# Performance work log

Measured on AMD Instinct MI355X. Metric: run time of the kernel, lower is better.

## Reference

```python
import jax, jax.numpy as jnp
import numpy as np

VOCAB, DIM, SEQ, DEPTH, WS, MULT = 32, 256, 8192, 6, 512, 4
BATCH = 2
NEG = -1e9  # mask fill value


def setup_inputs():
    key = jax.random.key(0)
    ks = jax.random.split(key, 8)
    L, d, h = DEPTH, DIM, DIM * MULT
    s = 0.02
    return {
        "tokens": jax.random.randint(ks[0], (BATCH, SEQ), 0, VOCAB),
        "embed": jax.random.normal(ks[1], (VOCAB, d)) * s,
        "ff_ln_s": jnp.ones((L, d)),
        "ff_ln_b": jnp.zeros((L, d)),
        "w1": jax.random.normal(ks[2], (L, d, h)) * s,
        "b1": jnp.zeros((L, h)),
        "w2": jax.random.normal(ks[3], (L, h, d)) * s,
        "b2": jnp.zeros((L, d)),
        "lnf_s": jnp.ones((d,)),
        "lnf_b": jnp.zeros((d,)),
        "w_out": jax.random.normal(ks[4], (d, VOCAB)) * s,
        "b_out": jnp.zeros((VOCAB,)),
    }


def layer_norm(x, s, b, eps=1e-5):
    m = jnp.mean(x, axis=-1, keepdims=True)
    v = jnp.var(x, axis=-1, keepdims=True)
    return (x - m) * jax.lax.rsqrt(v + eps) * s + b


def rotate_half(x):
    x1, x2 = jnp.split(x, 2, axis=-1)
    return jnp.concatenate([-x2, x1], axis=-1)


def local_attn(x, ws):
    # lucidrains LocalAttention: causal, look_backward=1, look_forward=0,
    # exact_windowsize=True, rotary pos emb on q/k. q = k = v = x (no projections).
    b, n, d = x.shape
    inv_freq = 1.0 / (10000.0 ** (jnp.arange(0, d, 2, dtype=jnp.float32) / d))
    t = jnp.arange(n, dtype=jnp.float32)
    fr = t[:, None] * inv_freq[None, :]
    fr = jnp.concatenate([fr, fr], axis=-1)  # (n, d)
    qk = x * jnp.cos(fr) + rotate_half(x) * jnp.sin(fr)  # rotary applied to q and k (identical)
    w = n // ws
    bq = qk.reshape(b, w, ws, d)
    bk = bq  # q == k here
    bv = x.reshape(b, w, ws, d)
    # look_around: each window sees [previous window, current window]
    pk = jnp.pad(bk, ((0, 0), (1, 0), (0, 0), (0, 0)))[:, :-1]
    pv = jnp.pad(bv, ((0, 0), (1, 0), (0, 0), (0, 0)))[:, :-1]
    bk2 = jnp.concatenate([pk, bk], axis=2)  # (b, w, 2*ws, d)
    bv2 = jnp.concatenate([pv, bv], axis=2)
    tq = jnp.arange(n).reshape(w, ws)
    tp = jnp.pad(tq, ((1, 0), (0, 0)), constant_values=-1)[:-1]
    tk = jnp.concatenate([tp, tq], axis=1)  # (w, 2*ws), -1 marks pad
    allowed = (
        (tk[:, None, :] >= 0)
        & (tq[:, :, None] >= tk[:, None, :])          # causal
        & (tq[:, :, None] <= tk[:, None, :] + ws)     # exact windowsize (look_backward=1)
    )
    sim = jnp.einsum("bwid,bwjd->bwij", bq, bk2) * (d ** -0.5)
    sim = jnp.where(allowed[None], sim, NEG)
    attn = jax.nn.softmax(sim, axis=-1)
    out = jnp.einsum("bwij,bwjd->bwid", attn, bv2)
    return out.reshape(b, n, d)


def reference(tokens, embed, ff_ln_s, ff_ln_b, w1, b1, w2, b2, lnf_s, lnf_b, w_out, b_out):
    x = embed[tokens]  # (b, n, d)
    for i in range(DEPTH):
        x = x + local_attn(x, WS)
        h = layer_norm(x, ff_ln_s[i], ff_ln_b[i])
        h = jax.nn.gelu(h @ w1[i] + b1[i], approximate=False)
        x = x + (h @ w2[i] + b2[i])
    return layer_norm(x, lnf_s, lnf_b) @ w_out + b_out  # (b, n, vocab)
```

## Files before the change

kernel.cpp:

```cpp
#include <hip/hip_runtime.h>
#include <hip/hip_bf16.h>
#include <math.h>

#define BATCH 2
#define SEQL 8192
#define DD 256
#define HDIM 1024
#define NLAYER 6
#define WSZ 512
#define NVOCAB 32
#define NTOK (BATCH*SEQL)
#define PLN (DD*HDIM)

typedef unsigned short u16;
typedef __attribute__((ext_vector_type(8))) short bf16x8;
typedef __attribute__((ext_vector_type(4))) float f32x4;

union B8 { uint4 u; bf16x8 b; ushort s[8]; uint w[4]; };

__device__ inline float bf2f(u16 v){
  unsigned int u = ((unsigned int)v) << 16;
  return __uint_as_float(u);
}
__device__ inline u16 f2bf(float f){
  unsigned int u = __float_as_uint(f);
  u += 0x7fff + ((u >> 16) & 1);
  return (u16)(u >> 16);
}

__device__ __forceinline__ void gload16(const void* g, void* l){
  __builtin_amdgcn_global_load_lds(
      (const __attribute__((address_space(1))) unsigned int*)g,
      (__attribute__((address_space(3))) unsigned int*)l, 16, 0, 0);
}

__global__ void k_tables(float* __restrict__ ct, float* __restrict__ st){
  int idx = blockIdx.x * 256 + threadIdx.x;
  if (idx >= SEQL * 128) return;
  int t = idx >> 7, i = idx & 127;
  float freq = expf(-((float)i / 128.0f) * 9.210340371976184f);
  float fr = (float)t * freq;
  ct[idx] = cosf(fr);
  st[idx] = sinf(fr);
}

__global__ void k_embed(const int* __restrict__ tokens, const float* __restrict__ emb,
                        float* __restrict__ x){
  int idx = blockIdx.x * 256 + threadIdx.x;
  int bt = idx >> 6, dv = (idx & 63) << 2;
  int tok = tokens[bt];
  *(float4*)(x + bt * DD + dv) = *(const float4*)(emb + tok * DD + dv);
}

__global__ void k_rope(const float* __restrict__ x, const float* __restrict__ ct,
                       const float* __restrict__ st, u16* __restrict__ qk,
                       u16* __restrict__ xv){
  int idx = blockIdx.x * 256 + threadIdx.x;
  int bt = idx >> 5, iv = (idx & 31) << 2;
  int t = bt & (SEQL - 1);
  const float* xr = x + bt * DD;
  float4 x1 = *(const float4*)(xr + iv);
  float4 x2 = *(const float4*)(xr + 128 + iv);
  float4 c = *(const float4*)(ct + t * 128 + iv);
  float4 s = *(const float4*)(st + t * 128 + iv);
  ushort4 q1, q2, v1, v2;
  q1.x = f2bf(x1.x * c.x - x2.x * s.x);  q2.x = f2bf(x2.x * c.x + x1.x * s.x);
  q1.y = f2bf(x1.y * c.y - x2.y * s.y);  q2.y = f2bf(x2.y * c.y + x1.y * s.y);
  q1.z = f2bf(x1.z * c.z - x2.z * s.z);  q2.z = f2bf(x2.z * c.z + x1.z * s.z);
  q1.w = f2bf(x1.w * c.w - x2.w * s.w);  q2.w = f2bf(x2.w * c.w + x1.w * s.w);
  v1.x = f2bf(x1.x); v1.y = f2bf(x1.y); v1.z = f2bf(x1.z); v1.w = f2bf(x1.w);
  v2.x = f2bf(x2.x); v2.y = f2bf(x2.y); v2.z = f2bf(x2.z); v2.w = f2bf(x2.w);
  *(ushort4*)(qk + bt * DD + iv)       = q1;
  *(ushort4*)(qk + bt * DD + 128 + iv) = q2;
  *(ushort4*)(xv + bt * DD + iv)       = v1;
  *(ushort4*)(xv + bt * DD + 128 + iv) = v2;
}

__global__ void __launch_bounds__(512, 2) k_attn2(const u16* __restrict__ qk,
                                                  const u16* __restrict__ xv,
                                                  const float* __restrict__ x,
                                                  float* __restrict__ y){
  __shared__ char smem[131072];
  float* redbuf = (float*)smem;

  const int tid = threadIdx.x;
  const int lane = tid & 63;
  const int w = tid >> 6;
  const int qh = w >> 1, kh = w & 1;
  const int l15 = lane & 15, lg = lane >> 4;

  const int qb = blockIdx.x * 64;
  const int t0 = qb & (SEQL - 1);
  const size_t bbase = (size_t)(qb >> 13) << 13;

  uint4 qf[8];
  {
    const u16* qr = qk + (size_t)(qb + qh*16 + l15) * DD + lg*4;
    #pragma unroll
    for (int s = 0; s < 8; ++s){
      uint2 a = *(const uint2*)(qr + s*32);
      uint2 b = *(const uint2*)(qr + s*32 + 16);
      qf[s] = make_uint4(a.x, a.y, b.x, b.y);
    }
  }

  f32x4 oacc[16];
  #pragma unroll
  for (int d = 0; d < 16; ++d) oacc[d] = (f32x4){0.f, 0.f, 0.f, 0.f};
  float lacc = 0.f;

  const int p0 = (t0 >= WSZ) ? (t0 - WSZ) : 0;
  const int ntile = ((t0 - p0) >> 6) + 1;

  const int sk15 = tid & 15, skt = (tid >> 4) & 3, sc = tid >> 6;
  const int sdh = tid & 31, sk0 = (tid >> 5) * 4;
  const int vkhw = sk0 >> 5, vh = (sk0 >> 4) & 1, vlgw = (sk0 >> 2) & 3;

  uint4 kreg[4];
  uint  vreg[4][4];

  {
    const u16* sb = qk + (bbase + (size_t)p0 + skt*16 + sk15) * DD;
    #pragma unroll
    for (int u = 0; u < 4; ++u) kreg[u] = *(const uint4*)(sb + u*64 + sc*8);
    #pragma unroll
    for (int u = 0; u < 4; ++u){
      int d0 = sdh*2 + u*64;
      const u16* vb = xv + (bbase + (size_t)p0 + sk0) * DD + d0;
      vreg[u][0] = *(const uint*)(vb);
      vreg[u][1] = *(const uint*)(vb + DD);
      vreg[u][2] = *(const uint*)(vb + 2*DD);
      vreg[u][3] = *(const uint*)(vb + 3*DD);
    }
  }
  #pragma unroll
  for (int u = 0; u < 4; ++u){
    int d0 = u*64 + sc*8;
    int s = d0 >> 5, r = d0 & 31;
    int h = r >> 4, lgw = (r & 15) >> 2;
    int rec = ((s*4 + skt)*4 + lgw)*16 + sk15;
    char* wp = smem + rec*16 + h*8;
    *(uint2*)wp         = make_uint2(kreg[u].x, kreg[u].y);
    *(uint2*)(wp + 256) = make_uint2(kreg[u].z, kreg[u].w);
  }
  #pragma unroll
  for (int u = 0; u < 4; ++u){
    int d0 = sdh*2 + u*64;
    uint a0 = vreg[u][0], a1 = vreg[u][1], a2 = vreg[u][2], a3 = vreg[u][3];
    uint w0 = (a0 & 0xffffu) | (a1 << 16);
    uint w1 = (a2 & 0xffffu) | (a3 << 16);
    uint w2 = (a0 >> 16) | (a1 & 0xffff0000u);
    uint w3 = (a2 >> 16) | (a3 & 0xffff0000u);
    int dimt = d0 >> 4, d15 = d0 & 15;
    int rec = ((dimt*2 + vkhw)*4 + vlgw)*16 + d15;
    char* wp = smem + 32768 + rec*16 + vh*8;
    *(uint2*)wp        = make_uint2(w0, w1);
    *(uint2*)(wp + 16) = make_uint2(w2, w3);
  }
  __syncthreads();

  int cur = 0;
  for (int ti = 0; ti < ntile; ++ti){
    const int p = p0 + ti*64;
    if (ti + 1 < ntile){
      const int pn = p + 64;
      const u16* sb = qk + (bbase + (size_t)pn + skt*16 + sk15) * DD;
      #pragma unroll
      for (int u = 0; u < 4; ++u) kreg[u] = *(const uint4*)(sb + u*64 + sc*8);
      #pragma unroll
      for (int u = 0; u < 4; ++u){
        int d0 = sdh*2 + u*64;
        const u16* vb = xv + (bbase + (size_t)pn + sk0) * DD + d0;
        vreg[u][0] = *(const uint*)(vb);
        vreg[u][1] = *(const uint*)(vb + DD);
        vreg[u][2] = *(const uint*)(vb + 2*DD);
        vreg[u][3] = *(const uint*)(vb + 3*DD);
      }
    }

    char* Klds = smem + cur*65536;
    char* Vlds = Klds + 32768;

    f32x4 sacc[2];
    sacc[0] = (f32x4){0.f,0.f,0.f,0.f};
    sacc[1] = (f32x4){0.f,0.f,0.f,0.f};
    #pragma unroll
    for (int s = 0; s < 8; ++s){
      B8 ka0, ka1, qbf;
      ka0.b = *(const bf16x8*)(Klds + (((s*4 + kh*2+0)*4 + lg)*16 + l15)*16);
      ka1.b = *(const bf16x8*)(Klds + (((s*4 + kh*2+1)*4 + lg)*16 + l15)*16);
      qbf.u = qf[s];
      sacc[0] = __builtin_amdgcn_mfma_f32_16x16x32_bf16(ka0.b, qbf.b, sacc[0], 0, 0, 0);
      sacc[1] = __builtin_amdgcn_mfma_f32_16x16x32_bf16(ka1.b, qbf.b, sacc[1], 0, 0, 0);
    }

    B8 pa;
    #pragma unroll
    for (int ktp = 0; ktp < 2; ++ktp){
      int kbase = p + kh*32 + ktp*16 + lg*4;
      int qpos = t0 + qh*16 + l15;
      #pragma unroll
      for (int r = 0; r < 4; ++r){
        int kpos = kbase + r;
        float sv = sacc[ktp][r] * 0.0625f;
        bool ok = (kpos <= qpos) && (qpos <= kpos + WSZ);
        float pv = ok ? __expf(sv) : 0.0f;
        lacc += pv;
        pa.s[ktp*4 + r] = f2bf(pv);
      }
    }

    #pragma unroll
    for (int dimt = 0; dimt < 16; ++dimt){
      B8 vb;
      vb.b = *(const bf16x8*)(Vlds + (((dimt*2 + kh)*4 + lg)*16 + l15)*16);
      oacc[dimt] = __builtin_amdgcn_mfma_f32_16x16x32_bf16(pa.b, vb.b, oacc[dimt], 0, 0, 0);
    }

    if (ti + 1 < ntile){
      char* nK = smem + (cur ^ 1)*65536;
      char* nV = nK + 32768;
      #pragma unroll
      for (int u = 0; u < 4; ++u){
        int d0 = u*64 + sc*8;
        int s = d0 >> 5, r = d0 & 31;
        int h = r >> 4, lgw = (r & 15) >> 2;
        int rec = ((s*4 + skt)*4 + lgw)*16 + sk15;
        char* wp = nK + rec*16 + h*8;
        *(uint2*)wp         = make_uint2(kreg[u].x, kreg[u].y);
        *(uint2*)(wp + 256) = make_uint2(kreg[u].z, kreg[u].w);
      }
      #pragma unroll
      for (int u = 0; u < 4; ++u){
        int d0 = sdh*2 + u*64;
        uint a0 = vreg[u][0], a1 = vreg[u][1], a2 = vreg[u][2], a3 = vreg[u][3];
        uint w0 = (a0 & 0xffffu) | (a1 << 16);
        uint w1 = (a2 & 0xffffu) | (a3 << 16);
        uint w2 = (a0 >> 16) | (a1 & 0xffff0000u);
        uint w3 = (a2 >> 16) | (a3 & 0xffff0000u);
        int dimt = d0 >> 4, d15 = d0 & 15;
        int rec = ((dimt*2 + vkhw)*4 + vlgw)*16 + d15;
        char* wp = nV + rec*16 + vh*8;
        *(uint2*)wp        = make_uint2(w0, w1);
        *(uint2*)(wp + 16) = make_uint2(w2, w3);
      }
    }
    __syncthreads();
    cur ^= 1;
  }

  lacc += __shfl_xor(lacc, 16, 64);
  lacc += __shfl_xor(lacc, 32, 64);
  if (lane < 16) redbuf[kh*64 + qh*16 + l15] = lacc;
  __syncthreads();
  if (tid < 64) redbuf[128 + tid] = redbuf[tid] + redbuf[64 + tid];
  __syncthreads();

  float* opass = redbuf + 192;
  #pragma unroll
  for (int pass = 0; pass < 8; ++pass){
    #pragma unroll
    for (int dt = 0; dt < 2; ++dt){
      int dimt = pass*2 + dt;
      #pragma unroll
      for (int r = 0; r < 4; ++r){
        int qrow = qh*16 + lg*4 + r;
        opass[(kh*64 + qrow)*36 + dt*16 + l15] = oacc[dimt][r];
      }
    }
    __syncthreads();
    {
      int q = tid >> 3, dv = (tid & 7) * 4;
      float4 o0 = *(float4*)&opass[q*36 + dv];
      float4 o1 = *(float4*)&opass[(64 + q)*36 + dv];
      float inv = 1.0f / redbuf[128 + q];
      size_t gi = (size_t)(qb + q) * DD + pass*32 + dv;
      float4 xr = *(const float4*)(x + gi);
      float4 ov;
      ov.x = xr.x + (o0.x + o1.x) * inv;
      ov.y = xr.y + (o0.y + o1.y) * inv;
      ov.z = xr.z + (o0.z + o1.z) * inv;
      ov.w = xr.w + (o0.w + o1.w) * inv;
      *(float4*)(y + gi) = ov;
    }
    __syncthreads();
  }
}

__global__ void __launch_bounds__(256) k_ln(const float* __restrict__ in,
                                            const float* __restrict__ g,
                                            const float* __restrict__ b,
                                            u16* __restrict__ out){
  int wid = (blockIdx.x * 256 + threadIdx.x) >> 6;
  int lane = threadIdx.x & 63;
  float4 v = *(const float4*)(in + wid * DD + lane * 4);
  float s = v.x + v.y + v.z + v.w;
  float ss = v.x * v.x + v.y * v.y + v.z * v.z + v.w * v.w;
  #pragma unroll
  for (int o = 32; o; o >>= 1){ s += __shfl_xor(s, o, 64); ss += __shfl_xor(ss, o, 64); }
  float m = s * (1.0f / DD);
  float var = ss * (1.0f / DD) - m * m;
  float rs = rsqrtf(var + 1e-5f);
  float4 gf = *(const float4*)(g + lane * 4);
  float4 bf = *(const float4*)(b + lane * 4);
  ushort4 o4;
  o4.x = f2bf((v.x - m) * rs * gf.x + bf.x);
  o4.y = f2bf((v.y - m) * rs * gf.y + bf.y);
  o4.z = f2bf((v.z - m) * rs * gf.z + bf.z);
  o4.w = f2bf((v.w - m) * rs * gf.w + bf.w);
  *(ushort4*)(out + wid * DD + lane * 4) = o4;
}

template<int KDIM, int NDIM>
__device__ __forceinline__ void split_one(const float* __restrict__ W,
                                          u16* __restrict__ Phi, int idx){
  int c15 = idx & 15;
  int lg = (idx >> 4) & 3;
  int nt = (idx >> 6) % (NDIM/16);
  int ks = idx / ((NDIM/16) * 64);
  int col = nt*16 + c15;
  B8 hi;
  #pragma unroll
  for (int j = 0; j < 8; ++j){
    int k = ks*32 + (j >> 2)*16 + lg*4 + (j & 3);
    hi.s[j] = f2bf(W[(size_t)k * NDIM + col]);
  }
  *(uint4*)(Phi + (size_t)idx * 8) = hi.u;
}

__global__ void __launch_bounds__(256) k_split2(const float* __restrict__ W1,
                                                const float* __restrict__ W2,
                                                u16* __restrict__ P){
  int b = blockIdx.x;
  if (b < 128) split_one<DD, HDIM>(W1, P, b*256 + threadIdx.x);
  else         split_one<HDIM, DD>(W2, P + PLN, (b - 128)*256 + threadIdx.x);
}

template<int KDIM, int NDIM, int EPI>
__global__ void __launch_bounds__(256, 4) k_gemm(const u16* __restrict__ A,
                                              const u16* __restrict__ BhG,
                                              const float* __restrict__ bias,
                                              const float* __restrict__ res,
                                              float* __restrict__ outf,
                                              u16* __restrict__ outh){
  __shared__ char smem[18432 + 8192];
  char* As = smem;
  char* Bs = smem + 18432;

  const int tid = threadIdx.x;
  const int lane = tid & 63;
  const int w = tid >> 6;
  const int wr = w >> 1, wc = w & 1;
  const int l15 = lane & 15, lg = lane >> 4;
  const int m0 = blockIdx.y * 128;
  const int n0 = blockIdx.x * 64;
  const int NT16 = NDIM / 16;

  f32x4 acc[4][2];
  #pragma unroll
  for (int a = 0; a < 4; ++a){
    acc[a][0] = (f32x4){0.f,0.f,0.f,0.f};
    acc[a][1] = (f32x4){0.f,0.f,0.f,0.f};
  }

  for (int kb = 0; kb < KDIM/64; ++kb){
    __syncthreads();
    #pragma unroll
    for (int p = 0; p < 4; ++p){
      int c = p*256 + tid;
      int row = c >> 3, cc = c & 7;
      uint4 v = *(const uint4*)(A + (size_t)(m0 + row) * KDIM + kb*64 + cc*8);
      *(uint4*)(As + row*144 + cc*16) = v;
    }
    #pragma unroll
    for (int p = 0; p < 2; ++p){
      int j = p*256 + tid;
      int chunk = j >> 6, r = j & 63;
      const u16* src = BhG
          + (((size_t)(kb*2 + (chunk >> 2)) * NT16 + (n0 >> 4) + (chunk & 3))*64 + r)*8;
      gload16(src, Bs + j*16);
    }
    __syncthreads();

    #pragma unroll
    for (int s = 0; s < 2; ++s){
      B8 af[4], bhf[2];
      #pragma unroll
      for (int a = 0; a < 4; ++a){
        const char* ab = As + (wr*64 + a*16 + l15)*144 + s*64 + lg*8;
        uint2 lo = *(const uint2*)ab;
        uint2 hi = *(const uint2*)(ab + 32);
        af[a].u = make_uint4(lo.x, lo.y, hi.x, hi.y);
      }
      #pragma unroll
      for (int c = 0; c < 2; ++c){
        int off = (((s*4 + wc*2 + c)*64) + lg*16 + l15)*16;
        bhf[c].u = *(const uint4*)(Bs + off);
      }
      #pragma unroll
      for (int a = 0; a < 4; ++a)
        #pragma unroll
        for (int c = 0; c < 2; ++c)
          acc[a][c] = __builtin_amdgcn_mfma_f32_16x16x32_bf16(af[a].b, bhf[c].b, acc[a][c], 0, 0, 0);
    }
  }

  float bv[2];
  bv[0] = bias[n0 + wc*32 + l15];
  bv[1] = bias[n0 + wc*32 + 16 + l15];

  #pragma unroll
  for (int a = 0; a < 4; ++a){
    #pragma unroll
    for (int c = 0; c < 2; ++c){
      #pragma unroll
      for (int r = 0; r < 4; ++r){
        int row = m0 + wr*64 + a*16 + lg*4 + r;
        int col = n0 + wc*32 + c*16 + l15;
        float v = acc[a][c][r] + bv[c];
        if (EPI == 0){
          float gl = 0.5f * v * (1.0f + erff(v * 0.70710678f));
          outh[(size_t)row * NDIM + col] = f2bf(gl);
        } else {
          outf[(size_t)row * NDIM + col] = v + res[(size_t)row * NDIM + col];
        }
      }
    }
  }
}

__global__ void __launch_bounds__(256) k_final(const float* __restrict__ x,
                                               const float* __restrict__ g,
                                               const float* __restrict__ b,
                                               const float* __restrict__ wout,
                                               const float* __restrict__ bout,
                                               float* __restrict__ out){
  __shared__ float lds[4][256];
  int widx = threadIdx.x >> 6, lane = threadIdx.x & 63;
  int bt = blockIdx.x * 4 + widx;
  float4 v = *(const float4*)(x + bt * DD + lane * 4);
  float s = v.x + v.y + v.z + v.w;
  float ss = v.x * v.x + v.y * v.y + v.z * v.z + v.w * v.w;
  #pragma unroll
  for (int o = 32; o; o >>= 1){ s += __shfl_xor(s, o, 64); ss += __shfl_xor(ss, o, 64); }
  float m = s * (1.0f / DD);
  float var = ss * (1.0f / DD) - m * m;
  float rs = rsqrtf(var + 1e-5f);
  float4 gf = *(const float4*)(g + lane * 4);
  float4 bf = *(const float4*)(b + lane * 4);
  lds[widx][lane * 4 + 0] = (v.x - m) * rs * gf.x + bf.x;
  lds[widx][lane * 4 + 1] = (v.y - m) * rs * gf.y + bf.y;
  lds[widx][lane * 4 + 2] = (v.z - m) * rs * gf.z + bf.z;
  lds[widx][lane * 4 + 3] = (v.w - m) * rs * gf.w + bf.w;
  __syncthreads();
  int vo = lane & 31, half = lane >> 5;
  const float* lp = &lds[widx][half * 128];
  const float* wp = wout + half * 128 * NVOCAB + vo;
  float acc = 0;
  #pragma unroll 4
  for (int d = 0; d < 128; ++d) acc += lp[d] * wp[d * NVOCAB];
  acc += __shfl_down(acc, 32, 64);
  if (lane < 32) out[bt * NVOCAB + vo] = acc + bout[vo];
}

extern "C" void kernel_launch(void* const* d_in, const int* in_sizes, int n_in,
                              void* d_out, int out_size, void* d_ws, size_t ws_size,
                              hipStream_t stream) {
  const int*   tokens = (const int*)d_in[0];
  const float* emb   = (const float*)d_in[1];
  const float* ffs   = (const float*)d_in[2];
  const float* ffb   = (const float*)d_in[3];
  const float* w1    = (const float*)d_in[4];
  const float* b1    = (const float*)d_in[5];
  const float* w2    = (const float*)d_in[6];
  const float* b2    = (const float*)d_in[7];
  const float* lnfs  = (const float*)d_in[8];
  const float* lnfb  = (const float*)d_in[9];
  const float* wout  = (const float*)d_in[10];
  const float* bout  = (const float*)d_in[11];
  float* out = (float*)d_out;

  char* ws = (char*)d_ws;
  float* x    = (float*)(ws);
  float* y    = (float*)(ws + (size_t)16*1024*1024);
  u16*   buf8 = (u16*)  (ws + (size_t)32*1024*1024);
  u16*   qk   = (u16*)  (ws + (size_t)40*1024*1024);
  u16*   h    = (u16*)  (ws + (size_t)48*1024*1024);
  float* ct   = (float*)(ws + (size_t)80*1024*1024);
  float* st   = (float*)(ws + (size_t)84*1024*1024);

  k_tables<<<4096, 256, 0, stream>>>(ct, st);
  k_embed<<<4096, 256, 0, stream>>>(tokens, emb, x);
  for (int L = 0; L < NLAYER; ++L){
    k_rope<<<2048, 256, 0, stream>>>(x, ct, st, qk, buf8);
    k_attn2<<<256, 512, 0, stream>>>(qk, buf8, x, y);
    k_ln  <<<4096, 256, 0, stream>>>(y, ffs + L*DD, ffb + L*DD, buf8);
    k_split2<<<256, 256, 0, stream>>>(w1 + (size_t)L*PLN, w2 + (size_t)L*PLN, qk);
    k_gemm<DD, HDIM, 0><<<dim3(16, 128), 256, 0, stream>>>(
        buf8, qk, b1 + L*HDIM, nullptr, nullptr, h);
    k_gemm<HDIM, DD, 1><<<dim3(4, 128), 256, 0, stream>>>(
        h, qk + PLN, b2 + L*DD, y, x, nullptr);
  }
  k_final<<<4096, 256, 0, stream>>>(x, lnfs, lnfb, wout, bout, out);
}
```

Before: 766.6 us.

## Fuse feed-forward LayerNorm into attention epilogue and remap attention block order

The attention kernel now computes row mean and variance of the residual output in its epilogue. It writes the normalized bf16 activations directly to a separate buffer, so the standalone LayerNorm launch and its re-read of y are skipped when the workspace is large enough. The block index is also permuted so that consecutive blocks are spread across sequence positions, which changes load balance across the varying tile counts. In exchange the kernel carries more live registers (eight float4 per thread) and adds a shuffle reduction, which may hurt occupancy.

```diff
diff --git a/kernel.cpp b/kernel.cpp
--- a/kernel.cpp
+++ b/kernel.cpp
@@ -79,7 +79,11 @@
 __global__ void __launch_bounds__(512, 2) k_attn2(const u16* __restrict__ qk,
                                                   const u16* __restrict__ xv,
                                                   const float* __restrict__ x,
-                                                  float* __restrict__ y){
+                                                  float* __restrict__ y,
+                                                  const float* __restrict__ g,
+                                                  const float* __restrict__ b,
+                                                  u16* __restrict__ lnx,
+                                                  int fuse){
   __shared__ char smem[131072];
   float* redbuf = (float*)smem;
 
@@ -89,7 +93,8 @@
   const int qh = w >> 1, kh = w & 1;
   const int l15 = lane & 15, lg = lane >> 4;
 
-  const int qb = blockIdx.x * 64;
+  const int qg = (blockIdx.x & 7) * 32 + (blockIdx.x >> 3);
+  const int qb = qg * 64;
   const int t0 = qb & (SEQL - 1);
   const size_t bbase = (size_t)(qb >> 13) << 13;
 
@@ -99,8 +104,8 @@
     #pragma unroll
     for (int s = 0; s < 8; ++s){
       uint2 a = *(const uint2*)(qr + s*32);
-      uint2 b = *(const uint2*)(qr + s*32 + 16);
-      qf[s] = make_uint4(a.x, a.y, b.x, b.y);
+      uint2 bq = *(const uint2*)(qr + s*32 + 16);
+      qf[s] = make_uint4(a.x, a.y, bq.x, bq.y);
     }
   }
 
@@ -256,6 +261,10 @@
   if (tid < 64) redbuf[128 + tid] = redbuf[tid] + redbuf[64 + tid];
   __syncthreads();
 
+  const int q = tid >> 3, dv = (tid & 7) * 4;
+  float4 ovs[8];
+  float lsum = 0.f, lss = 0.f;
+
   float* opass = redbuf + 192;
   #pragma unroll
   for (int pass = 0; pass < 8; ++pass){
@@ -270,7 +279,6 @@
     }
     __syncthreads();
     {
-      int q = tid >> 3, dv = (tid & 7) * 4;
       float4 o0 = *(float4*)&opass[q*36 + dv];
       float4 o1 = *(float4*)&opass[(64 + q)*36 + dv];
       float inv = 1.0f / redbuf[128 + q];
@@ -282,8 +290,33 @@
       ov.z = xr.z + (o0.z + o1.z) * inv;
       ov.w = xr.w + (o0.w + o1.w) * inv;
       *(float4*)(y + gi) = ov;
+      ovs[pass] = ov;
+      lsum += ov.x + ov.y + ov.z + ov.w;
+      lss  += ov.x*ov.x + ov.y*ov.y + ov.z*ov.z + ov.w*ov.w;
     }
     __syncthreads();
+  }
+
+  if (fuse){
+    #pragma unroll
+    for (int o = 1; o < 8; o <<= 1){
+      lsum += __shfl_xor(lsum, o, 64);
+      lss  += __shfl_xor(lss,  o, 64);
+    }
+    float m = lsum * (1.0f / DD);
+    float var = lss * (1.0f / DD) - m * m;
+    float rs = rsqrtf(var + 1e-5f);
+    #pragma unroll
+    for (int pass = 0; pass < 8; ++pass){
+      float4 gf = *(const float4*)(g + pass*32 + dv);
+      float4 bf = *(const float4*)(b + pass*32 + dv);
+      ushort4 o4;
+      o4.x = f2bf((ovs[pass].x - m) * rs * gf.x + bf.x);
+      o4.y = f2bf((ovs[pass].y - m) * rs * gf.y + bf.y);
+      o4.z = f2bf((ovs[pass].z - m) * rs * gf.z + bf.z);
+      o4.w = f2bf((ovs[pass].w - m) * rs * gf.w + bf.w);
+      *(ushort4*)(lnx + (size_t)(qb + q) * DD + pass*32 + dv) = o4;
+    }
   }
 }
 
@@ -489,15 +522,21 @@
   float* ct   = (float*)(ws + (size_t)80*1024*1024);
   float* st   = (float*)(ws + (size_t)84*1024*1024);
 
+  const int fuse = (ws_size >= (size_t)96*1024*1024) ? 1 : 0;
+  u16* lnx = fuse ? (u16*)(ws + (size_t)88*1024*1024)
+                  : buf8;
+
   k_tables<<<4096, 256, 0, stream>>>(ct, st);
   k_embed<<<4096, 256, 0, stream>>>(tokens, emb, x);
   for (int L = 0; L < NLAYER; ++L){
     k_rope<<<2048, 256, 0, stream>>>(x, ct, st, qk, buf8);
-    k_attn2<<<256, 512, 0, stream>>>(qk, buf8, x, y);
-    k_ln  <<<4096, 256, 0, stream>>>(y, ffs + L*DD, ffb + L*DD, buf8);
+    k_attn2<<<256, 512, 0, stream>>>(qk, buf8, x, y,
+                                     ffs + L*DD, ffb + L*DD, lnx, fuse);
+    if (!fuse)
+      k_ln<<<4096, 256, 0, stream>>>(y, ffs + L*DD, ffb + L*DD, lnx);
     k_split2<<<256, 256, 0, stream>>>(w1 + (size_t)L*PLN, w2 + (size_t)L*PLN, qk);
     k_gemm<DD, HDIM, 0><<<dim3(16, 128), 256, 0, stream>>>(
-        buf8, qk, b1 + L*HDIM, nullptr, nullptr, h);
+        lnx, qk, b1 + L*HDIM, nullptr, nullptr, h);
     k_gemm<HDIM, DD, 1><<<dim3(4, 128), 256, 0, stream>>>(
         h, qk + PLN, b2 + L*DD, y, x, nullptr);
   }
```

Measured after the change: 711.5 us. 1.08x faster.
